# Optimization experiments

Measured on AMD Instinct MI355X. Metric: run time of the kernel, lower is better.

The kernel has to match this reference:

```python
import jax, jax.numpy as jnp
import numpy as np

H = 32        # num_attention_heads (query heads)
G = 8         # num_query_groups (KV heads)
D = 128       # head_dim
HID = 4096    # hidden_size
THETA = 10000.0


def _rope(x, pos):
    # x: [B, h, S, D]; pos: [S]. Rotate-half (LLaMA) convention.
    half = D // 2
    inv_freq = 1.0 / (THETA ** (jnp.arange(0, half, dtype=jnp.float32) / half))
    ang = pos[:, None].astype(jnp.float32) * inv_freq[None, :]   # [S, half]
    cos = jnp.cos(ang)[None, None]                               # [1,1,S,half]
    sin = jnp.sin(ang)[None, None]
    x1, x2 = x[..., :half], x[..., half:]
    return jnp.concatenate([x1 * cos - x2 * sin, x1 * sin + x2 * cos], axis=-1)


def setup_inputs() -> dict:
    key = jax.random.key(0)
    ks = jax.random.split(key, 9)
    s = 0.02
    return {
        "hidden_states": jax.random.normal(ks[0], (1, 2048, HID), jnp.float32),
        "Wq": jax.random.normal(ks[1], (HID, H * D), jnp.float32) * s,
        "bq": jnp.zeros((H * D,), jnp.float32),
        "Wk": jax.random.normal(ks[2], (HID, G * D), jnp.float32) * s,
        "bk": jnp.zeros((G * D,), jnp.float32),
        "Wv": jax.random.normal(ks[3], (HID, G * D), jnp.float32) * s,
        "bv": jnp.zeros((G * D,), jnp.float32),
        "Wo": jax.random.normal(ks[4], (H * D, HID), jnp.float32) * s,
        "bo": jnp.zeros((HID,), jnp.float32),
    }


def reference(hidden_states, Wq, bq, Wk, bk, Wv, bv, Wo, bo):
    B, S, _ = hidden_states.shape
    R = H // G  # query heads per KV group

    q = hidden_states @ Wq + bq  # [B,S,H*D]
    k = hidden_states @ Wk + bk  # [B,S,G*D]
    v = hidden_states @ Wv + bv  # [B,S,G*D]

    q = q.reshape(B, S, H, D).transpose(0, 2, 1, 3)  # [B,H,S,D]
    k = k.reshape(B, S, G, D).transpose(0, 2, 1, 3)  # [B,G,S,D]
    v = v.reshape(B, S, G, D).transpose(0, 2, 1, 3)  # [B,G,S,D]

    pos = jnp.arange(S)
    q = _rope(q, pos)
    k = _rope(k, pos)

    # Grouped attention: broadcast KV across the R query heads of each group
    qg = q.reshape(B, G, R, S, D)
    scores = jnp.einsum('bgrsd,bgtd->bgrst', qg, k) / jnp.sqrt(jnp.float32(D))
    causal = jnp.tril(jnp.ones((S, S), dtype=bool))
    scores = jnp.where(causal[None, None, None], scores, jnp.finfo(scores.dtype).min)
    probs = jax.nn.softmax(scores, axis=-1)
    ctx = jnp.einsum('bgrst,bgtd->bgrsd', probs, v)          # [B,G,R,S,D]
    ctx = ctx.reshape(B, H, S, D).transpose(0, 2, 1, 3).reshape(B, S, H * D)
    return ctx @ Wo + bo
```

## Files before the change

### kernel.cpp

```cpp
#include <hip/hip_runtime.h>
#include <hip/hip_bf16.h>
#include <math.h>

#define HID   4096
#define NH    32
#define NG    8
#define DH    128
#define SEQ   2048
#define QKV_N 6144
#define KOFF  4096
#define VOFF  5120

typedef __bf16 bf16x8 __attribute__((ext_vector_type(8)));
typedef float  f32x4  __attribute__((ext_vector_type(4)));
using bf16 = __hip_bfloat16;

#define LOG2E 1.4426950408889634f
#define SCALE 0.08838834764831845f

typedef const __attribute__((address_space(1))) void* gas_p;
typedef __attribute__((address_space(3))) void* las_p;
__device__ __forceinline__ void async_copy16(void* lds, const void* g) {
  __builtin_amdgcn_global_load_lds((gas_p)g, (las_p)lds, 16, 0, 0);
}

__device__ __forceinline__ unsigned pack2(float a, float b) {
  union { bf16 h[2]; unsigned u; } t;
  t.h[0] = __float2bfloat16(a);
  t.h[1] = __float2bfloat16(b);
  return t.u;
}

__global__ __launch_bounds__(256) void prepass_kernel(const float* __restrict__ X,
                                                      const float* __restrict__ Wq, const float* __restrict__ Wk,
                                                      const float* __restrict__ Wv, const float* __restrict__ Wo,
                                                      const float* __restrict__ bq, const float* __restrict__ bk,
                                                      const float* __restrict__ bv,
                                                      bf16* __restrict__ Xb,
                                                      bf16* __restrict__ Wqkv_t, bf16* __restrict__ Wot,
                                                      float* __restrict__ bqkv) {
  const int bx = blockIdx.x, by = blockIdx.y;
  const int t = threadIdx.x;
  if (bx >= 288) {
    if (by < 24) {
      int i = by * 256 + t;
      if (i < 4096)       bqkv[i] = bq[i];
      else if (i < 5120)  bqkv[i] = bk[i - 4096];
      else                bqkv[i] = bv[i - 5120];
    }
    return;
  }
  if (bx >= 160) {
    int i = ((bx - 160) + 128 * by) * 256 + t;
    float4 v = ((const float4*)X)[i];
    union { bf16 h[4]; uint2 u; } c;
    c.h[0] = __float2bfloat16(v.x);
    c.h[1] = __float2bfloat16(v.y);
    c.h[2] = __float2bfloat16(v.z);
    c.h[3] = __float2bfloat16(v.w);
    ((uint2*)Xb)[i] = c.u;
    return;
  }
  __shared__ bf16 T[64][72];
  const float* W; bf16* dst; int N, ntile;
  if (bx < 64)      { W = Wq; dst = Wqkv_t;                      N = 4096; ntile = bx; }
  else if (bx < 80) { W = Wk; dst = Wqkv_t + (size_t)KOFF * HID; N = 1024; ntile = bx - 64; }
  else if (bx < 96) { W = Wv; dst = Wqkv_t + (size_t)VOFF * HID; N = 1024; ntile = bx - 80; }
  else              { W = Wo; dst = Wot;                         N = 4096; ntile = bx - 96; }
  const int n0 = ntile * 64, k0 = by * 64;
  const int nn = (t & 15) * 4, kk = t >> 4;
#pragma unroll
  for (int p = 0; p < 4; ++p) {
    const int k = kk + p * 16;
    float4 v = *(const float4*)&W[(size_t)(k0 + k) * N + n0 + nn];
    union { bf16 h[4]; uint2 u; } c;
    c.h[0] = __float2bfloat16(v.x);
    c.h[1] = __float2bfloat16(v.y);
    c.h[2] = __float2bfloat16(v.z);
    c.h[3] = __float2bfloat16(v.w);
    *(uint2*)&T[k][nn] = c.u;
  }
  __syncthreads();
  const int kc = t & 7, nr = t >> 3;
#pragma unroll
  for (int p = 0; p < 2; ++p) {
    const int n = nr + p * 32;
    union { bf16 h[8]; uint4 u; } o;
#pragma unroll
    for (int i = 0; i < 8; ++i) o.h[i] = T[kc * 8 + i][n];
    *(uint4*)&dst[(size_t)(n0 + n) * HID + k0 + kc * 8] = o.u;
  }
}

__device__ __forceinline__ void st_out(float* C, size_t idx, float v) { C[idx] = v; }
__device__ __forceinline__ void st_out(bf16*  C, size_t idx, float v) { C[idx] = __float2bfloat16(v); }

template <int BM, typename OutT>
__global__ __launch_bounds__(512, 2) void gemm_pipe_kernel(const bf16* __restrict__ A, const bf16* __restrict__ Bt,
                                                           const float* __restrict__ bias, OutT* __restrict__ C,
                                                           int M, int N, int K) {
  constexpr int MT   = BM / 32;
  constexpr int CA64 = BM / 16;
  constexpr int LPT  = (BM + 256) / 128;

  __shared__ alignas(16) bf16 As[4][BM * 32];
  __shared__ alignas(16) bf16 Bs[4][256 * 32];

  const int tid  = threadIdx.x;
  const int w    = tid >> 6, lane = tid & 63, quad = lane >> 4, l16 = lane & 15;
  const int wr   = w >> 2, wc = w & 3;
  const int m0   = blockIdx.y * BM, n0 = blockIdx.x * 256;

  const bf16* const Ag = A  + (size_t)m0 * K;
  const bf16* const Bg = Bt + (size_t)n0 * K;

  auto stage = [&](int kst, int buf) {
    const int k0 = kst * 32;
#pragma unroll
    for (int i = 0; i < LPT; ++i) {
      const int seg = i * 8 + w;
      if (i < CA64 / 8) {
        const int c  = seg * 64 + lane;
        const int r  = c >> 2;
        const int gq = (c & 3) ^ ((r >> 1) & 3);
        async_copy16(&As[buf][seg * 512], Ag + (size_t)r * K + k0 + gq * 8);
      } else {
        const int sb = seg - CA64;
        const int c  = sb * 64 + lane;
        const int r  = c >> 2;
        const int gq = (c & 3) ^ ((r >> 1) & 3);
        async_copy16(&Bs[buf][sb * 512], Bg + (size_t)r * K + k0 + gq * 8);
      }
    }
  };

  auto wait_2L = [&]() {
    if constexpr (BM == 256) asm volatile("s_waitcnt vmcnt(8)" ::: "memory");
    else                     asm volatile("s_waitcnt vmcnt(6)" ::: "memory");
  };

  f32x4 acc[MT][4];
  f32x4 zero4 = {0.f, 0.f, 0.f, 0.f};
#pragma unroll
  for (int mt = 0; mt < MT; ++mt)
#pragma unroll
    for (int nt = 0; nt < 4; ++nt) acc[mt][nt] = zero4;

  const int nst = K >> 5;

  stage(0, 0);
  stage(1, 1);
  stage(2, 2);
  wait_2L();
  __builtin_amdgcn_s_barrier();
  asm volatile("" ::: "memory");

  for (int s = 0; s < nst; ++s) {
    const int buf = s & 3;
    const bf16* Ab = &As[buf][0];
    const bf16* Bb = &Bs[buf][0];

    bf16x8 bfr[4];
#pragma unroll
    for (int nt = 0; nt < 4; ++nt) {
      const int Rn = wc * 64 + nt * 16 + l16;
      bfr[nt] = *(const bf16x8*)&Bb[Rn * 32 + ((quad ^ ((Rn >> 1) & 3)) << 3)];
    }

    const int t = s + 3;
    stage(t < nst ? t : nst - 1, t & 3);

    __builtin_amdgcn_s_setprio(1);
#pragma unroll
    for (int mt = 0; mt < MT; ++mt) {
      const int Rm = wr * (BM / 2) + mt * 16 + l16;
      bf16x8 af = *(const bf16x8*)&Ab[Rm * 32 + ((quad ^ ((Rm >> 1) & 3)) << 3)];
#pragma unroll
      for (int nt = 0; nt < 4; ++nt)
        acc[mt][nt] = __builtin_amdgcn_mfma_f32_16x16x32_bf16(af, bfr[nt], acc[mt][nt], 0, 0, 0);
    }
    __builtin_amdgcn_s_setprio(0);

    wait_2L();
    __builtin_amdgcn_s_barrier();
    asm volatile("" ::: "memory");
  }

#pragma unroll
  for (int nt = 0; nt < 4; ++nt) {
    const int col = n0 + wc * 64 + nt * 16 + l16;
    const float bv = bias[col];
#pragma unroll
    for (int mt = 0; mt < MT; ++mt) {
#pragma unroll
      for (int r = 0; r < 4; ++r) {
        const int row = m0 + wr * (BM / 2) + mt * 16 + quad * 4 + r;
        st_out(C, (size_t)row * N + col, acc[mt][nt][r] + bv);
      }
    }
  }
}

__global__ __launch_bounds__(256) void rope_vtrans_kernel(bf16* __restrict__ qkv, bf16* __restrict__ vt) {
  __shared__ bf16 tle[32][33];
  const int bx = blockIdx.x;
  const int tid = threadIdx.x;
  if (bx < 2560) {
    int t = bx * 256 + tid;
    int c  = t & 7;
    int hs = (t >> 3) % 40;
    int s  = t / 320;
    int base = (hs < 32) ? hs * 128 : KOFF + (hs - 32) * 128;
    bf16* p = qkv + (size_t)s * QKV_N + base + c * 8;
    union { bf16x8 v; bf16 h[8]; } a, b, ra, rb;
    a.v = *(bf16x8*)p;
    b.v = *(bf16x8*)(p + 64);
#pragma unroll
    for (int j = 0; j < 8; ++j) {
      int d = c * 8 + j;
      float inv = expf(d * -0.14391156862f);
      float ang = (float)s * inv;
      float sn, cs;
      sincosf(ang, &sn, &cs);
      float x1 = __bfloat162float(a.h[j]);
      float x2 = __bfloat162float(b.h[j]);
      ra.h[j] = __float2bfloat16(x1 * cs - x2 * sn);
      rb.h[j] = __float2bfloat16(x1 * sn + x2 * cs);
    }
    *(bf16x8*)p        = ra.v;
    *(bf16x8*)(p + 64) = rb.v;
  } else {
    const int b = bx - 2560;
    const int s0 = (b & 63) * 32, d0 = ((b >> 6) & 3) * 32, g = b >> 8;
    const int tx = tid & 31, ty = tid >> 5;
#pragma unroll
    for (int i = 0; i < 4; ++i)
      tle[ty + i * 8][tx] = qkv[(size_t)(s0 + ty + i * 8) * QKV_N + VOFF + g * 128 + d0 + tx];
    __syncthreads();
#pragma unroll
    for (int i = 0; i < 4; ++i)
      vt[(size_t)(g * 128 + d0 + ty + i * 8) * SEQ + s0 + tx] = tle[tx][ty + i * 8];
  }
}

__global__ __launch_bounds__(512, 4) void attn_kernel(const bf16* __restrict__ qkv, const bf16* __restrict__ vt,
                                                      bf16* __restrict__ ctx) {
  __shared__ alignas(16) bf16 Ks[2][2][32][128];
  __shared__ alignas(16) bf16 Vs[2][2][64][64];
  __shared__ float rs1[64];
  float* const red = (float*)&Ks[0][0][0][0];

  const int bx = blockIdx.x;
  const int h  = blockIdx.y;
  const int g  = h >> 2;
  const int tid = threadIdx.x;
  const int w = tid >> 6;
  const int gid = w >> 2, wq = w & 3;
  const int lane = tid & 63, quad = lane >> 4, l16 = lane & 15;

  const float c1 = SCALE * LOG2E;
  const float c2 = 12.0f * LOG2E;

  const int addrA = (((quad & 1) << 5) + l16) * 4;
  const int addrB = addrA + 64;
  const bool hiq = quad >= 2;

  f32x4 zero4 = {0.f, 0.f, 0.f, 0.f};

  auto stage = [&](int kt2, int buf) {
    const int ktg = 2 * kt2 + gid;
    const bf16* kg = qkv + (size_t)(ktg * 32) * QKV_N + KOFF + g * 128;
    const bf16* vg = vt + (size_t)(g * 128) * SEQ + ktg * 32;
#pragma unroll
    for (int i = 0; i < 2; ++i) {
      const int c = (i * 4 + wq) * 64 + lane;
      {
        const int key = c >> 4, j = c & 15;
        const int js = (j & 8) | ((j ^ key) & 7);
        async_copy16(&Ks[gid][buf][0][0] + (size_t)(i * 4 + wq) * 512,
                     kg + (size_t)key * QKV_N + js * 8);
      }
      {
        const int row = c >> 3, d = row * 2 + ((c >> 2) & 1), k8s = c & 3;
        const int vjs = (k8s ^ row) & 3;
        async_copy16(&Vs[gid][buf][0][0] + (size_t)(i * 4 + wq) * 512,
                     vg + (size_t)d * SEQ + vjs * 8);
      }
    }
  };

  for (int ph = 0; ph < 2; ++ph) {
    const int qt = ph ? bx : (31 - bx);

    bf16x8 qf[4];
    {
      const bf16* qp = qkv + (size_t)(qt * 64 + wq * 16 + l16) * QKV_N + h * 128 + quad * 8;
#pragma unroll
      for (int ks = 0; ks < 4; ++ks) qf[ks] = *(const bf16x8*)(qp + ks * 32);
    }

    f32x4 o[8];
#pragma unroll
    for (int dt = 0; dt < 8; ++dt) o[dt] = zero4;
    float rsum = 0.f;

    __syncthreads();
    stage(0, 0);

    for (int kt2 = 0; kt2 <= qt; ++kt2) {
      const int cur = kt2 & 1;
      __syncthreads();
      if (kt2 + 1 <= qt) stage(kt2 + 1, 1 - cur);

      f32x4 s[2];
#pragma unroll
      for (int nt = 0; nt < 2; ++nt) {
        s[nt] = zero4;
#pragma unroll
        for (int ks = 0; ks < 4; ++ks) {
          const int ch = ks * 4 + quad;
          bf16x8 kf = *(const bf16x8*)&Ks[gid][cur][nt * 16 + l16][((ch & 8) | ((ch ^ l16) & 7)) * 8];
          s[nt] = __builtin_amdgcn_mfma_f32_16x16x32_bf16(kf, qf[ks], s[nt], 0, 0, 0);
        }
      }

#pragma unroll
      for (int nt = 0; nt < 2; ++nt)
#pragma unroll
        for (int r = 0; r < 4; ++r)
          s[nt][r] = exp2f(fmaf(s[nt][r], c1, -c2));

      if (kt2 == qt) {
        const int koff = gid * 32;
        const int q_local = wq * 16 + l16;
#pragma unroll
        for (int nt = 0; nt < 2; ++nt)
#pragma unroll
          for (int r = 0; r < 4; ++r)
            if (koff + nt * 16 + quad * 4 + r > q_local) s[nt][r] = 0.f;
      }

      rsum += (s[0][0] + s[0][1]) + (s[0][2] + s[0][3]) +
              (s[1][0] + s[1][1]) + (s[1][2] + s[1][3]);

      unsigned pk[2][2];
#pragma unroll
      for (int nt = 0; nt < 2; ++nt) {
        pk[nt][0] = pack2(s[nt][0], s[nt][1]);
        pk[nt][1] = pack2(s[nt][2], s[nt][3]);
      }
      int a0l = __builtin_amdgcn_ds_bpermute(addrA, (int)pk[0][0]);
      int a1l = __builtin_amdgcn_ds_bpermute(addrA, (int)pk[0][1]);
      int b0l = __builtin_amdgcn_ds_bpermute(addrB, (int)pk[0][0]);
      int b1l = __builtin_amdgcn_ds_bpermute(addrB, (int)pk[0][1]);
      int a0h = __builtin_amdgcn_ds_bpermute(addrA, (int)pk[1][0]);
      int a1h = __builtin_amdgcn_ds_bpermute(addrA, (int)pk[1][1]);
      int b0h = __builtin_amdgcn_ds_bpermute(addrB, (int)pk[1][0]);
      int b1h = __builtin_amdgcn_ds_bpermute(addrB, (int)pk[1][1]);
      union { int u[4]; bf16x8 v; } pf;
      pf.u[0] = hiq ? a0h : a0l;
      pf.u[1] = hiq ? a1h : a1l;
      pf.u[2] = hiq ? b0h : b0l;
      pf.u[3] = hiq ? b1h : b1l;

#pragma unroll
      for (int dt = 0; dt < 8; ++dt) {
        const int d = dt * 16 + l16, row = d >> 1;
        const int slot = (quad ^ row) & 3;
        bf16x8 vf = *(const bf16x8*)&Vs[gid][cur][row][(d & 1) * 32 + slot * 8];
        o[dt] = __builtin_amdgcn_mfma_f32_16x16x32_bf16(vf, pf.v, o[dt], 0, 0, 0);
      }
    }

    rsum += __shfl_xor(rsum, 16, 64);
    rsum += __shfl_xor(rsum, 32, 64);

    __syncthreads();
    if (gid == 1) {
#pragma unroll
      for (int dt = 0; dt < 8; ++dt)
        *(f32x4*)&red[(((wq * 8 + dt) * 64) + lane) * 4] = o[dt];
      if (quad == 0) rs1[wq * 16 + l16] = rsum;
    }
    __syncthreads();
    if (gid == 0) {
      const float inv = 1.0f / (rsum + rs1[wq * 16 + l16]);
      const int srow = qt * 64 + wq * 16 + l16;
      bf16* cp = ctx + (size_t)srow * HID + h * 128 + quad * 4;
#pragma unroll
      for (int dt = 0; dt < 8; ++dt) {
        f32x4 sum = o[dt] + *(const f32x4*)&red[(((wq * 8 + dt) * 64) + lane) * 4];
        union { bf16 hh[4]; uint2 u; } ov;
#pragma unroll
        for (int r = 0; r < 4; ++r) ov.hh[r] = __float2bfloat16(sum[r] * inv);
        *(uint2*)(cp + dt * 16) = ov.u;
      }
    }
  }
}

extern "C" void kernel_launch(void* const* d_in, const int* in_sizes, int n_in,
                              void* d_out, int out_size, void* d_ws, size_t ws_size,
                              hipStream_t stream) {
  const float* X  = (const float*)d_in[0];
  const float* Wq = (const float*)d_in[1];
  const float* bq = (const float*)d_in[2];
  const float* Wk = (const float*)d_in[3];
  const float* bk = (const float*)d_in[4];
  const float* Wv = (const float*)d_in[5];
  const float* bv = (const float*)d_in[6];
  const float* Wo = (const float*)d_in[7];
  const float* bo = (const float*)d_in[8];
  float* out = (float*)d_out;

  char* ws = (char*)d_ws;
  size_t off = 0;
  auto alloc = [&](size_t bytes) { char* p = ws + off; off += (bytes + 255) & ~255ULL; return p; };
  bf16*  Xb     = (bf16*) alloc((size_t)SEQ * HID * 2);
  bf16*  Wqkv_t = (bf16*) alloc((size_t)QKV_N * HID * 2);
  bf16*  Wot    = (bf16*) alloc((size_t)HID * HID * 2);
  float* bqkv   = (float*)alloc((size_t)QKV_N * 4);
  bf16*  QKV    = (bf16*) alloc((size_t)SEQ * QKV_N * 2);
  bf16*  Vt     = (bf16*) alloc((size_t)NG * DH * SEQ * 2);
  bf16*  Ctx    = (bf16*) alloc((size_t)SEQ * HID * 2);

  prepass_kernel<<<dim3(289, 64), 256, 0, stream>>>(X, Wq, Wk, Wv, Wo, bq, bk, bv,
                                                    Xb, Wqkv_t, Wot, bqkv);
  gemm_pipe_kernel<256, bf16><<<dim3(QKV_N / 256, SEQ / 256), 512, 0, stream>>>(Xb, Wqkv_t, bqkv, QKV, SEQ, QKV_N, HID);
  rope_vtrans_kernel<<<2560 + 2048, 256, 0, stream>>>(QKV, Vt);
  attn_kernel<<<dim3(16, NH), 512, 0, stream>>>(QKV, Vt, Ctx);
  gemm_pipe_kernel<128, float><<<dim3(HID / 256, SEQ / 128), 512, 0, stream>>>(Ctx, Wot, bo, out, SEQ, HID, HID);
}
```

Measured before the change: 567.0 us.

## Restructure GEMM mainloop into eight-phase double-buffered schedule with interleaved loads

Replaces the 4-stage, 32-wide-K ring buffer in both projection GEMMs with a 2-buffer, 64-wide-K scheme. Each K step is split into four phases, and each phase issues a slice of the next tile's global-to-LDS copies between its fragment reads and its MFMAs. The goal is finer interleaving of memory traffic with compute and a shallower wait count. The cost is more barriers per K step and less prefetch depth, which may expose load latency.

Measured after the change: 501.1 us. -11.6%, faster.

```diff
diff --git a/kernel.cpp b/kernel.cpp
--- a/kernel.cpp
+++ b/kernel.cpp
@@ -96,106 +96,128 @@
 __device__ __forceinline__ void st_out(bf16*  C, size_t idx, float v) { C[idx] = __float2bfloat16(v); }
 
 template <int BM, typename OutT>
-__global__ __launch_bounds__(512, 2) void gemm_pipe_kernel(const bf16* __restrict__ A, const bf16* __restrict__ Bt,
-                                                           const float* __restrict__ bias, OutT* __restrict__ C,
-                                                           int M, int N, int K) {
-  constexpr int MT   = BM / 32;
-  constexpr int CA64 = BM / 16;
-  constexpr int LPT  = (BM + 256) / 128;
-
-  __shared__ alignas(16) bf16 As[4][BM * 32];
-  __shared__ alignas(16) bf16 Bs[4][256 * 32];
-
-  const int tid  = threadIdx.x;
-  const int w    = tid >> 6, lane = tid & 63, quad = lane >> 4, l16 = lane & 15;
-  const int wr   = w >> 2, wc = w & 3;
-  const int m0   = blockIdx.y * BM, n0 = blockIdx.x * 256;
+__global__ __launch_bounds__(512, 2) void gemm8_kernel(const bf16* __restrict__ A, const bf16* __restrict__ Bt,
+                                                       const float* __restrict__ bias, OutT* __restrict__ C,
+                                                       int M, int N, int K) {
+  constexpr int MT = BM / 32;
+  constexpr int LA = (BM * 32 * 2) / (512 * 16);
+  constexpr int LB = 2;
+
+  __shared__ alignas(16) bf16 As[2][2][BM * 32];
+  __shared__ alignas(16) bf16 Bs[2][2][256 * 32];
+
+  const int tid = threadIdx.x;
+  const int w = tid >> 6, lane = tid & 63, quad = lane >> 4, l16 = lane & 15;
+  const int wr = w >> 2, wc = w & 3;
+  const int m0 = blockIdx.y * BM, n0 = blockIdx.x * 256;
 
   const bf16* const Ag = A  + (size_t)m0 * K;
   const bf16* const Bg = Bt + (size_t)n0 * K;
 
-  auto stage = [&](int kst, int buf) {
-    const int k0 = kst * 32;
-#pragma unroll
-    for (int i = 0; i < LPT; ++i) {
-      const int seg = i * 8 + w;
-      if (i < CA64 / 8) {
-        const int c  = seg * 64 + lane;
-        const int r  = c >> 2;
-        const int gq = (c & 3) ^ ((r >> 1) & 3);
-        async_copy16(&As[buf][seg * 512], Ag + (size_t)r * K + k0 + gq * 8);
-      } else {
-        const int sb = seg - CA64;
-        const int c  = sb * 64 + lane;
-        const int r  = c >> 2;
-        const int gq = (c & 3) ^ ((r >> 1) & 3);
-        async_copy16(&Bs[buf][sb * 512], Bg + (size_t)r * K + k0 + gq * 8);
-      }
-    }
-  };
-
-  auto wait_2L = [&]() {
-    if constexpr (BM == 256) asm volatile("s_waitcnt vmcnt(8)" ::: "memory");
-    else                     asm volatile("s_waitcnt vmcnt(6)" ::: "memory");
+  auto stA = [&](int skt, int db, int kh) {
+    const int kb = skt * 64 + kh * 32;
+#pragma unroll
+    for (int L = 0; L < LA; ++L) {
+      const int cib = (L * 8 + w) * 64;
+      const int ci  = cib + lane;
+      const int r   = ci >> 2;
+      const int j   = (ci & 3) ^ ((r >> 1) & 3);
+      async_copy16(&As[db][kh][cib * 8], Ag + (size_t)r * K + kb + j * 8);
+    }
+  };
+  auto stB = [&](int skt, int db, int kh) {
+    const int kb = skt * 64 + kh * 32;
+#pragma unroll
+    for (int L = 0; L < LB; ++L) {
+      const int cib = (L * 8 + w) * 64;
+      const int ci  = cib + lane;
+      const int r   = ci >> 2;
+      const int j   = (ci & 3) ^ ((r >> 1) & 3);
+      async_copy16(&Bs[db][kh][cib * 8], Bg + (size_t)r * K + kb + j * 8);
+    }
+  };
+
+  auto waitv = [&]() {
+    if constexpr (BM == 256) asm volatile("s_waitcnt vmcnt(4)" ::: "memory");
+    else                     asm volatile("s_waitcnt vmcnt(3)" ::: "memory");
+  };
+
+  bf16x8 af[MT], bf2[2];
+  auto ldA = [&](int buf, int kh) {
+#pragma unroll
+    for (int mf = 0; mf < MT; ++mf) {
+      const int r = wr * (BM / 2) + mf * 16 + l16;
+      af[mf] = *(const bf16x8*)&As[buf][kh][r * 32 + ((quad ^ ((r >> 1) & 3)) << 3)];
+    }
+  };
+  auto ldB = [&](int buf, int kh, int ph) {
+#pragma unroll
+    for (int j = 0; j < 2; ++j) {
+      const int r = wc * 64 + (ph * 2 + j) * 16 + l16;
+      bf2[j] = *(const bf16x8*)&Bs[buf][kh][r * 32 + ((quad ^ ((r >> 1) & 3)) << 3)];
+    }
   };
 
   f32x4 acc[MT][4];
   f32x4 zero4 = {0.f, 0.f, 0.f, 0.f};
 #pragma unroll
-  for (int mt = 0; mt < MT; ++mt)
-#pragma unroll
-    for (int nt = 0; nt < 4; ++nt) acc[mt][nt] = zero4;
-
-  const int nst = K >> 5;
-
-  stage(0, 0);
-  stage(1, 1);
-  stage(2, 2);
-  wait_2L();
+  for (int mf = 0; mf < MT; ++mf)
+#pragma unroll
+    for (int nf = 0; nf < 4; ++nf) acc[mf][nf] = zero4;
+
+#define GPHASE(BUF, KH, PH, STAGE_CALL)                                                     \
+  do {                                                                                      \
+    if (PH == 0) ldA(BUF, KH);                                                              \
+    ldB(BUF, KH, PH);                                                                       \
+    STAGE_CALL;                                                                             \
+    __builtin_amdgcn_s_barrier();                                                           \
+    asm volatile("s_waitcnt lgkmcnt(0)" ::: "memory");                                      \
+    __builtin_amdgcn_sched_barrier(0);                                                      \
+    __builtin_amdgcn_s_setprio(1);                                                          \
+    _Pragma("unroll")                                                                       \
+    for (int mf = 0; mf < MT; ++mf) {                                                       \
+      acc[mf][PH * 2 + 0] =                                                                 \
+          __builtin_amdgcn_mfma_f32_16x16x32_bf16(af[mf], bf2[0], acc[mf][PH * 2 + 0], 0, 0, 0); \
+      acc[mf][PH * 2 + 1] =                                                                 \
+          __builtin_amdgcn_mfma_f32_16x16x32_bf16(af[mf], bf2[1], acc[mf][PH * 2 + 1], 0, 0, 0); \
+    }                                                                                       \
+    __builtin_amdgcn_s_setprio(0);                                                          \
+    waitv();                                                                                \
+    __builtin_amdgcn_s_barrier();                                                           \
+    asm volatile("" ::: "memory");                                                          \
+  } while (0)
+
+  const int KT = K >> 6;
+
+  stA(0, 0, 0); stB(0, 0, 0); stA(0, 0, 1); stB(0, 0, 1);
+  waitv();
   __builtin_amdgcn_s_barrier();
   asm volatile("" ::: "memory");
 
-  for (int s = 0; s < nst; ++s) {
-    const int buf = s & 3;
-    const bf16* Ab = &As[buf][0];
-    const bf16* Bb = &Bs[buf][0];
-
-    bf16x8 bfr[4];
-#pragma unroll
-    for (int nt = 0; nt < 4; ++nt) {
-      const int Rn = wc * 64 + nt * 16 + l16;
-      bfr[nt] = *(const bf16x8*)&Bb[Rn * 32 + ((quad ^ ((Rn >> 1) & 3)) << 3)];
-    }
-
-    const int t = s + 3;
-    stage(t < nst ? t : nst - 1, t & 3);
-
-    __builtin_amdgcn_s_setprio(1);
-#pragma unroll
-    for (int mt = 0; mt < MT; ++mt) {
-      const int Rm = wr * (BM / 2) + mt * 16 + l16;
-      bf16x8 af = *(const bf16x8*)&Ab[Rm * 32 + ((quad ^ ((Rm >> 1) & 3)) << 3)];
-#pragma unroll
-      for (int nt = 0; nt < 4; ++nt)
-        acc[mt][nt] = __builtin_amdgcn_mfma_f32_16x16x32_bf16(af, bfr[nt], acc[mt][nt], 0, 0, 0);
-    }
-    __builtin_amdgcn_s_setprio(0);
-
-    wait_2L();
-    __builtin_amdgcn_s_barrier();
-    asm volatile("" ::: "memory");
-  }
-
-#pragma unroll
-  for (int nt = 0; nt < 4; ++nt) {
-    const int col = n0 + wc * 64 + nt * 16 + l16;
+  for (int kt = 0; kt < KT; ++kt) {
+    const int buf = kt & 1;
+    const int nkt = kt + 1;
+    const int skt = nkt < KT ? nkt : KT - 1;
+    const int db  = nkt & 1;
+    GPHASE(buf, 0, 0, stA(skt, db, 0));
+    GPHASE(buf, 0, 1, stB(skt, db, 0));
+    GPHASE(buf, 1, 0, stA(skt, db, 1));
+    GPHASE(buf, 1, 1, stB(skt, db, 1));
+  }
+#undef GPHASE
+
+  asm volatile("s_waitcnt vmcnt(0)" ::: "memory");
+
+#pragma unroll
+  for (int nf = 0; nf < 4; ++nf) {
+    const int col = n0 + wc * 64 + nf * 16 + l16;
     const float bv = bias[col];
 #pragma unroll
-    for (int mt = 0; mt < MT; ++mt) {
+    for (int mf = 0; mf < MT; ++mf) {
 #pragma unroll
       for (int r = 0; r < 4; ++r) {
-        const int row = m0 + wr * (BM / 2) + mt * 16 + quad * 4 + r;
-        st_out(C, (size_t)row * N + col, acc[mt][nt][r] + bv);
+        const int row = m0 + wr * (BM / 2) + mf * 16 + quad * 4 + r;
+        st_out(C, (size_t)row * N + col, acc[mf][nf][r] + bv);
       }
     }
   }
@@ -426,8 +448,8 @@
 
   prepass_kernel<<<dim3(289, 64), 256, 0, stream>>>(X, Wq, Wk, Wv, Wo, bq, bk, bv,
                                                     Xb, Wqkv_t, Wot, bqkv);
-  gemm_pipe_kernel<256, bf16><<<dim3(QKV_N / 256, SEQ / 256), 512, 0, stream>>>(Xb, Wqkv_t, bqkv, QKV, SEQ, QKV_N, HID);
+  gemm8_kernel<256, bf16><<<dim3(QKV_N / 256, SEQ / 256), 512, 0, stream>>>(Xb, Wqkv_t, bqkv, QKV, SEQ, QKV_N, HID);
   rope_vtrans_kernel<<<2560 + 2048, 256, 0, stream>>>(QKV, Vt);
   attn_kernel<<<dim3(16, NH), 512, 0, stream>>>(QKV, Vt, Ctx);
-  gemm_pipe_kernel<128, float><<<dim3(HID / 256, SEQ / 128), 512, 0, stream>>>(Ctx, Wot, bo, out, SEQ, HID, HID);
-}
+  gemm8_kernel<128, float><<<dim3(HID / 256, SEQ / 128), 512, 0, stream>>>(Ctx, Wot, bo, out, SEQ, HID, HID);
+}
```
